# Kernel tuning notes

Hardware: AMD Instinct MI355X
Metric: run time of the kernel (lower is better)

The kernel has to match this reference:

```python
import jax, jax.numpy as jnp
import numpy as np

NUM_ITERATIONS = 3


def _squash_over_classes(s):
    # s: [B, C, O]; original squashes over dim=2 of [B,1,C,O,1] == the class dim C
    norm_sqr = jnp.sum(s * s, axis=1, keepdims=True)          # [B,1,O]
    scale = jnp.sqrt(norm_sqr) + 1e-10
    mag = norm_sqr / (1.0 + norm_sqr)
    return s * mag / scale


def setup_inputs() -> dict:
    key = jax.random.key(0)
    k1, k2 = jax.random.split(key)
    B, K, I, C, O = 256, 8, 1152, 10, 16
    x = jax.random.normal(k1, (B, K, I), dtype=jnp.float32)
    weights = jax.random.normal(k2, (I, C, O, K), dtype=jnp.float32)
    return {"x": x, "weights": weights}


def reference(x, weights):
    # x: [B, K, I]; weights: [I, C, O, K]
    B = x.shape[0]
    I, C = weights.shape[0], weights.shape[1]
    u = jnp.swapaxes(x, 1, 2)                                  # [B, I, K]
    # prediction vectors u_hat_{j|i}: [B, I, C, O]
    u_j_i = jnp.einsum('icok,bik->bico', weights, u)
    b = jnp.zeros((I, C), dtype=x.dtype)                       # routing logits (shared over batch)
    out = None
    for _ in range(NUM_ITERATIONS):
        c = jax.nn.softmax(b, axis=0)                          # softmax over input capsules I
        s = jnp.einsum('ic,bico->bco', c, u_j_i)               # weighted sum over I -> [B, C, O]
        out = _squash_over_classes(s)                          # [B, C, O]
        # agreement: <u_hat, v>, mean over batch -> [I, C]
        agr = jnp.einsum('bico,bco->ic', u_j_i, out) / B
        b = b + agr
    return out[..., None]                                      # [B, C, O, 1] matches out.squeeze(1)
```

## Files before the change

kernel.cpp:

```cpp
#include <hip/hip_runtime.h>

#define B 256
#define KDIM 8
#define IDIM 1152
#define CDIM 10
#define CO 160
#define IK 9216
#define NPART 6
#define AIT 6

typedef __bf16 bf16x8 __attribute__((ext_vector_type(8)));
typedef unsigned short ushort8 __attribute__((ext_vector_type(8)));
typedef float f32x4 __attribute__((ext_vector_type(4)));

__device__ __forceinline__ unsigned short f2bf(float f) {
  unsigned u = __float_as_uint(f);
  unsigned r = u + 0x7fff + ((u >> 16) & 1);
  return (unsigned short)(r >> 16);
}

union U8B8 { ushort8 u; bf16x8 h; };


__global__ void __launch_bounds__(256) k_prep(const float* __restrict__ x,
                                              const float* __restrict__ W,
                                              unsigned short* __restrict__ XbP,
                                              unsigned short* __restrict__ XkP,
                                              unsigned short* __restrict__ WqP,
                                              float* __restrict__ logits) {
  const int bid = blockIdx.x;
  const int t = threadIdx.x;
  if (bid < 288) {
    __shared__ float tf[KDIM * 1056];
    const int i0 = (bid % 36) * 32;
    const int b0 = (bid / 36) * 32;
    const int tx = t & 31, ty = t >> 5;
#pragma unroll
    for (int r = 0; r < 4; ++r) {
      int b = b0 + ty + r * 8;
#pragma unroll
      for (int k = 0; k < 8; ++k)
        tf[k * 1056 + (ty + r * 8) * 33 + tx] =
            x[((size_t)b * KDIM + k) * IDIM + i0 + tx];
    }
    __syncthreads();
#pragma unroll
    for (int r = 0; r < 4; ++r) {
      int idx = r * 256 + t;
      int bth = idx >> 9, kc8 = (idx >> 6) & 7, lq = (idx >> 4) & 3, lr = idx & 15;
      ushort8 v;
#pragma unroll
      for (int e = 0; e < 8; ++e)
        v[e] = f2bf(tf[e * 1056 + (bth * 16 + lr) * 33 + kc8 * 4 + lq]);
      int bt = (b0 >> 4) + bth;
      int kc = (i0 >> 2) + kc8;
      *reinterpret_cast<ushort8*>(
          &XbP[(((size_t)bt * 288 + kc) * 64 + lq * 16 + lr) * 8]) = v;
    }
    {
      const int bh = b0 >> 6, kc = (b0 >> 5) & 1;
#pragma unroll
      for (int r = 0; r < 4; ++r) {
        int idx = r * 256 + t;
        int il = idx >> 5, k = (idx >> 2) & 7, lql = idx & 3;
        int i = i0 + il;
        int bx = i / 6, r6 = i - bx * 6;
        int w = r6 >> 1, lr = (r6 & 1) * 8 + k;
        ushort8 v;
#pragma unroll
        for (int e = 0; e < 8; ++e)
          v[e] = f2bf(tf[k * 1056 + (lql * 8 + e) * 33 + il]);
        *reinterpret_cast<ushort8*>(
            &XkP[((((size_t)(bx * 3 + w) * 4 + bh) * 2 + kc) * 64 + lql * 16 + lr) * 8]) = v;
      }
    }
  } else {
    const int bz = bid - 288;
    const int i0 = bz * 16;
    const int ii = t >> 4, lr = t & 15;
    const int i = i0 + ii;
    const int kc = i >> 2, lq = i & 3;
#pragma unroll
    for (int c = 0; c < CDIM; ++c) {
      const float* src = &W[(size_t)i * 1280 + c * 128 + lr * 8];
      float4 w0 = *(const float4*)src;
      float4 w1 = *(const float4*)(src + 4);
      ushort8 v;
      v[0] = f2bf(w0.x); v[1] = f2bf(w0.y); v[2] = f2bf(w0.z); v[3] = f2bf(w0.w);
      v[4] = f2bf(w1.x); v[5] = f2bf(w1.y); v[6] = f2bf(w1.z); v[7] = f2bf(w1.w);
      *reinterpret_cast<ushort8*>(
          &WqP[(((size_t)c * 288 + kc) * 64 + lq * 16 + lr) * 8]) = v;
    }
    if (bz < 45) logits[bz * 256 + t] = 0.f;
  }
}

template <bool UNI>
__global__ void __launch_bounds__(256) k_s(const float* __restrict__ logits,
                                           const unsigned short* __restrict__ WqP,
                                           const unsigned short* __restrict__ XbP,
                                           float* __restrict__ s_part) {
  const int c = blockIdx.x, bt4 = blockIdx.y, g = blockIdx.z;
  const int t = threadIdx.x, w = t >> 6, l = t & 63;
  const int lr = l & 15, lq = l >> 4;
  const int s = g * 4 + w;

  __shared__ float red[3 * 1088];

  float qreg[12];
  if constexpr (UNI) {
#pragma unroll
    for (int t9 = 0; t9 < 12; ++t9) qreg[t9] = 1.f / (float)IDIM;
  } else {
    __shared__ float cls[IDIM];
    __shared__ float red4[4];
    float m = -1e30f;
    for (int i = t; i < IDIM; i += 256) {
      float v = logits[i * CDIM + c];
      cls[i] = v;
      m = fmaxf(m, v);
    }
#pragma unroll
    for (int off = 32; off; off >>= 1) m = fmaxf(m, __shfl_xor(m, off));
    if ((t & 63) == 0) red4[t >> 6] = m;
    __syncthreads();
    m = fmaxf(fmaxf(red4[0], red4[1]), fmaxf(red4[2], red4[3]));
    __syncthreads();
    float ps = 0.f;
    for (int i = t; i < IDIM; i += 256) {
      float e = expf(cls[i] - m);
      cls[i] = e;
      ps += e;
    }
#pragma unroll
    for (int off = 32; off; off >>= 1) ps += __shfl_xor(ps, off);
    if ((t & 63) == 0) red4[t >> 6] = ps;
    __syncthreads();
    const float rinv = 1.f / (red4[0] + red4[1] + red4[2] + red4[3]);
#pragma unroll
    for (int t9 = 0; t9 < 12; ++t9)
      qreg[t9] = cls[(s * 12 + t9) * 4 + lq] * rinv;
  }

  f32x4 acc[4];
#pragma unroll
  for (int j = 0; j < 4; ++j) acc[j] = (f32x4){0.f, 0.f, 0.f, 0.f};

  const unsigned short* Ap  = &WqP[(size_t)c * 147456 + l * 8];
  const unsigned short* Bp0 = &XbP[(size_t)(bt4 * 4 + 0) * 147456 + l * 8];
  const unsigned short* Bp1 = &XbP[(size_t)(bt4 * 4 + 1) * 147456 + l * 8];
  const unsigned short* Bp2 = &XbP[(size_t)(bt4 * 4 + 2) * 147456 + l * 8];
  const unsigned short* Bp3 = &XbP[(size_t)(bt4 * 4 + 3) * 147456 + l * 8];

#pragma unroll 4
  for (int t9 = 0; t9 < 12; ++t9) {
    const int off = (s * 12 + t9) * 512;
    ushort8 av = *reinterpret_cast<const ushort8*>(Ap + off);
    U8B8 b0; b0.u = *reinterpret_cast<const ushort8*>(Bp0 + off);
    U8B8 b1; b1.u = *reinterpret_cast<const ushort8*>(Bp1 + off);
    U8B8 b2; b2.u = *reinterpret_cast<const ushort8*>(Bp2 + off);
    U8B8 b3; b3.u = *reinterpret_cast<const ushort8*>(Bp3 + off);
    U8B8 a;
#pragma unroll
    for (int e = 0; e < 8; ++e) {
      float f = __uint_as_float((unsigned)av[e] << 16) * qreg[t9];
      a.u[e] = f2bf(f);
    }
    acc[0] = __builtin_amdgcn_mfma_f32_16x16x32_bf16(a.h, b0.h, acc[0], 0, 0, 0);
    acc[1] = __builtin_amdgcn_mfma_f32_16x16x32_bf16(a.h, b1.h, acc[1], 0, 0, 0);
    acc[2] = __builtin_amdgcn_mfma_f32_16x16x32_bf16(a.h, b2.h, acc[2], 0, 0, 0);
    acc[3] = __builtin_amdgcn_mfma_f32_16x16x32_bf16(a.h, b3.h, acc[3], 0, 0, 0);
  }

  if (w) {
#pragma unroll
    for (int j = 0; j < 4; ++j)
#pragma unroll
      for (int j2 = 0; j2 < 4; ++j2)
        red[(w - 1) * 1088 + l * 17 + j * 4 + j2] = acc[j][j2];
  }
  __syncthreads();
  if (w == 0) {
#pragma unroll
    for (int r = 0; r < 3; ++r)
#pragma unroll
      for (int j = 0; j < 4; ++j)
#pragma unroll
        for (int j2 = 0; j2 < 4; ++j2)
          acc[j][j2] += red[r * 1088 + l * 17 + j * 4 + j2];
#pragma unroll
    for (int j = 0; j < 4; ++j)
#pragma unroll
      for (int j2 = 0; j2 < 4; ++j2)
        s_part[((size_t)g * B + bt4 * 64 + j * 16 + lr) * CO + c * 16 + lq * 4 + j2] =
            acc[j][j2];
  }
}

__global__ void __launch_bounds__(256) k_sqm(const float* __restrict__ s_part,
                                             unsigned short* __restrict__ outP) {
  const int t = threadIdx.x;
  const int b0 = blockIdx.x * 8;
  __shared__ float sq[8][160];
  __shared__ float fo[8][16];
  float vv[8];
  if (t < CO) {
#pragma unroll
    for (int bi = 0; bi < 8; ++bi) {
      float sv = 0.f;
#pragma unroll
      for (int p = 0; p < NPART; ++p)
        sv += s_part[((size_t)p * B + b0 + bi) * CO + t];
      vv[bi] = sv;
      sq[bi][t] = sv * sv;
    }
  }
  __syncthreads();
  if (t < 128) {
    int bi = t >> 4, o = t & 15;
    float ns = 0.f;
#pragma unroll
    for (int c = 0; c < CDIM; ++c) ns += sq[bi][c * 16 + o];
    fo[bi][o] = (ns / (1.f + ns)) / (sqrtf(ns) + 1e-10f);
  }
  __syncthreads();
  if (t < CO) {
    const int nt = t >> 4, lr = t & 15;
    const int bh = b0 >> 6, kc = (b0 >> 5) & 1, lq = (b0 >> 3) & 3;
    ushort8 v;
#pragma unroll
    for (int bi = 0; bi < 8; ++bi) v[bi] = f2bf(vv[bi] * fo[bi][t & 15]);
    *reinterpret_cast<ushort8*>(
        &outP[((((size_t)bh * 10 + nt) * 2 + kc) * 4 + lq) * 128 + lr * 8]) = v;
  }
}

__global__ void __launch_bounds__(256) k_sqf(const float* __restrict__ s_part,
                                             float* __restrict__ out) {
  const int t = threadIdx.x;
  const int b0 = blockIdx.x * 8;
  __shared__ float sq[8][160];
  __shared__ float fo[8][16];
  float vv[8];
  if (t < CO) {
#pragma unroll
    for (int bi = 0; bi < 8; ++bi) {
      float sv = 0.f;
#pragma unroll
      for (int p = 0; p < NPART; ++p)
        sv += s_part[((size_t)p * B + b0 + bi) * CO + t];
      vv[bi] = sv;
      sq[bi][t] = sv * sv;
    }
  }
  __syncthreads();
  if (t < 128) {
    int bi = t >> 4, o = t & 15;
    float ns = 0.f;
#pragma unroll
    for (int c = 0; c < CDIM; ++c) ns += sq[bi][c * 16 + o];
    fo[bi][o] = (ns / (1.f + ns)) / (sqrtf(ns) + 1e-10f);
  }
  __syncthreads();
  if (t < CO) {
#pragma unroll
    for (int bi = 0; bi < 8; ++bi)
      out[(size_t)(b0 + bi) * CO + t] = vv[bi] * fo[bi][t & 15];
  }
}

__global__ void __launch_bounds__(256) k_agr(const float* __restrict__ W,
                                             const unsigned short* __restrict__ XkP,
                                             const unsigned short* __restrict__ outP,
                                             float* __restrict__ logits) {
  const int bx = blockIdx.x;
  const int bh = blockIdx.y;
  const int t = threadIdx.x, w = t >> 6, l = t & 63;
  const int lr = l & 15, lq = l >> 4;
  __shared__ __align__(16) float yl[CO][52];

  if (w < 3) {
    f32x4 acc[10];
#pragma unroll
    for (int nt = 0; nt < 10; ++nt) acc[nt] = (f32x4){0.f, 0.f, 0.f, 0.f};
    const unsigned short* Ap = &XkP[(((size_t)(bx * 3 + w) * 4 + bh) * 1024) + l * 8];
    const unsigned short* Bp = &outP[(size_t)bh * 10240 + l * 8];
#pragma unroll
    for (int kc = 0; kc < 2; ++kc) {
      U8B8 a; a.u = *reinterpret_cast<const ushort8*>(Ap + kc * 512);
#pragma unroll
      for (int nt = 0; nt < 10; ++nt) {
        U8B8 bv;
        bv.u = *reinterpret_cast<const ushort8*>(Bp + nt * 1024 + kc * 512);
        acc[nt] = __builtin_amdgcn_mfma_f32_16x16x32_bf16(a.h, bv.h, acc[nt], 0, 0, 0);
      }
    }
#pragma unroll
    for (int nt = 0; nt < 10; ++nt)
#pragma unroll
      for (int j = 0; j < 4; ++j)
        yl[nt * 16 + lr][w * 16 + lq * 4 + j] = acc[nt][j];
  }
  __syncthreads();

  if (t < 120) {
    const int ii = t / 20, rem = t % 20, cc = rem >> 1, oh = rem & 1;
    const float* Wp = &W[((size_t)(bx * AIT + ii) * CDIM + cc) * 128 + oh * 64];
    float sum = 0.f;
#pragma unroll
    for (int o = 0; o < 8; ++o) {
      float4 w0 = *(const float4*)(&Wp[o * 8]);
      float4 w1 = *(const float4*)(&Wp[o * 8 + 4]);
      const float* yr = &yl[cc * 16 + oh * 8 + o][ii * 8];
      float4 y0 = *(const float4*)(&yr[0]);
      float4 y1 = *(const float4*)(&yr[4]);
      sum += w0.x * y0.x + w0.y * y0.y + w0.z * y0.z + w0.w * y0.w
           + w1.x * y1.x + w1.y * y1.y + w1.z * y1.z + w1.w * y1.w;
    }
    sum += __shfl_xor(sum, 1);
    if (oh == 0)
      atomicAdd(&logits[(bx * AIT + ii) * CDIM + cc], sum * (1.f / (float)B));
  }
}

extern "C" void kernel_launch(void* const* d_in, const int* in_sizes, int n_in,
                              void* d_out, int out_size, void* d_ws, size_t ws_size,
                              hipStream_t stream) {
  const float* x = (const float*)d_in[0];
  const float* W = (const float*)d_in[1];
  float* out = (float*)d_out;

  float* logits = (float*)d_ws;
  float* s_part = logits + IDIM * CDIM;
  unsigned short* XbP = (unsigned short*)(s_part + (size_t)NPART * B * CO);
  unsigned short* XkP = XbP + (size_t)B * IK;
  unsigned short* WqP = XkP + (size_t)IK * B;
  unsigned short* outP = WqP + (size_t)CO * IK;

  k_prep<<<360, 256, 0, stream>>>(x, W, XbP, XkP, WqP, logits);

  for (int it = 0; it < 3; ++it) {
    if (it == 0)
      k_s<true><<<dim3(CDIM, 4, NPART), 256, 0, stream>>>(logits, WqP, XbP, s_part);
    else
      k_s<false><<<dim3(CDIM, 4, NPART), 256, 0, stream>>>(logits, WqP, XbP, s_part);
    if (it < 2) {
      k_sqm<<<32, 256, 0, stream>>>(s_part, outP);
      k_agr<<<dim3(IDIM / AIT, 4), 256, 0, stream>>>(W, XkP, outP, logits);
    } else {
      k_sqf<<<32, 256, 0, stream>>>(s_part, out);
    }
  }
}
```

Before: 68.28 us.

## Fuse squash into k_s via last-block atomic counter; prescale weights by 1/I

```diff
diff --git a/kernel.cpp b/kernel.cpp
--- a/kernel.cpp
+++ b/kernel.cpp
@@ -20,6 +20,16 @@
 }
 
 union U8B8 { ushort8 u; bf16x8 h; };
+union U64F2 { unsigned long long u; float f[2]; };
+
+__device__ __forceinline__ void st64_llc(void* p, unsigned long long v) {
+  __hip_atomic_store((unsigned long long*)p, v, __ATOMIC_RELAXED,
+                     __HIP_MEMORY_SCOPE_AGENT);
+}
+__device__ __forceinline__ unsigned long long ld64_llc(const void* p) {
+  return __hip_atomic_load((unsigned long long*)p, __ATOMIC_RELAXED,
+                           __HIP_MEMORY_SCOPE_AGENT);
+}
 
 
 __global__ void __launch_bounds__(256) k_prep(const float* __restrict__ x,
@@ -27,7 +37,8 @@
                                               unsigned short* __restrict__ XbP,
                                               unsigned short* __restrict__ XkP,
                                               unsigned short* __restrict__ WqP,
-                                              float* __restrict__ logits) {
+                                              float* __restrict__ logits,
+                                              int* __restrict__ cnt) {
   const int bid = blockIdx.x;
   const int t = threadIdx.x;
   if (bid < 288) {
@@ -80,40 +91,46 @@
     const int ii = t >> 4, lr = t & 15;
     const int i = i0 + ii;
     const int kc = i >> 2, lq = i & 3;
+    const float sc = 1.f / (float)IDIM;
 #pragma unroll
     for (int c = 0; c < CDIM; ++c) {
       const float* src = &W[(size_t)i * 1280 + c * 128 + lr * 8];
       float4 w0 = *(const float4*)src;
       float4 w1 = *(const float4*)(src + 4);
       ushort8 v;
-      v[0] = f2bf(w0.x); v[1] = f2bf(w0.y); v[2] = f2bf(w0.z); v[3] = f2bf(w0.w);
-      v[4] = f2bf(w1.x); v[5] = f2bf(w1.y); v[6] = f2bf(w1.z); v[7] = f2bf(w1.w);
+      v[0] = f2bf(w0.x * sc); v[1] = f2bf(w0.y * sc);
+      v[2] = f2bf(w0.z * sc); v[3] = f2bf(w0.w * sc);
+      v[4] = f2bf(w1.x * sc); v[5] = f2bf(w1.y * sc);
+      v[6] = f2bf(w1.z * sc); v[7] = f2bf(w1.w * sc);
       *reinterpret_cast<ushort8*>(
           &WqP[(((size_t)c * 288 + kc) * 64 + lq * 16 + lr) * 8]) = v;
     }
     if (bz < 45) logits[bz * 256 + t] = 0.f;
-  }
-}
-
-template <bool UNI>
+    if (bz == 45 && t < 16) cnt[t] = 0;
+  }
+}
+
+template <int MODE>
 __global__ void __launch_bounds__(256) k_s(const float* __restrict__ logits,
                                            const unsigned short* __restrict__ WqP,
                                            const unsigned short* __restrict__ XbP,
-                                           float* __restrict__ s_part) {
+                                           float* __restrict__ s_part,
+                                           unsigned short* __restrict__ outP,
+                                           float* __restrict__ out,
+                                           int* __restrict__ cnt) {
   const int c = blockIdx.x, bt4 = blockIdx.y, g = blockIdx.z;
   const int t = threadIdx.x, w = t >> 6, l = t & 63;
   const int lr = l & 15, lq = l >> 4;
   const int s = g * 4 + w;
 
-  __shared__ float red[3 * 1088];
+  __shared__ __align__(16) unsigned char smem[45064];
+  float* red = (float*)(smem) + IDIM + 4;
+  int* islast = (int*)(smem + 45056);
 
   float qreg[12];
-  if constexpr (UNI) {
-#pragma unroll
-    for (int t9 = 0; t9 < 12; ++t9) qreg[t9] = 1.f / (float)IDIM;
-  } else {
-    __shared__ float cls[IDIM];
-    __shared__ float red4[4];
+  if constexpr (MODE != 0) {
+    float* cls = (float*)smem;
+    float* red4 = cls + IDIM;
     float m = -1e30f;
     for (int i = t; i < IDIM; i += 256) {
       float v = logits[i * CDIM + c];
@@ -136,10 +153,11 @@
     for (int off = 32; off; off >>= 1) ps += __shfl_xor(ps, off);
     if ((t & 63) == 0) red4[t >> 6] = ps;
     __syncthreads();
-    const float rinv = 1.f / (red4[0] + red4[1] + red4[2] + red4[3]);
+    const float rinv = (float)IDIM / (red4[0] + red4[1] + red4[2] + red4[3]);
 #pragma unroll
     for (int t9 = 0; t9 < 12; ++t9)
       qreg[t9] = cls[(s * 12 + t9) * 4 + lq] * rinv;
+    __syncthreads();
   }
 
   f32x4 acc[4];
@@ -161,10 +179,14 @@
     U8B8 b2; b2.u = *reinterpret_cast<const ushort8*>(Bp2 + off);
     U8B8 b3; b3.u = *reinterpret_cast<const ushort8*>(Bp3 + off);
     U8B8 a;
-#pragma unroll
-    for (int e = 0; e < 8; ++e) {
-      float f = __uint_as_float((unsigned)av[e] << 16) * qreg[t9];
-      a.u[e] = f2bf(f);
+    if constexpr (MODE == 0) {
+      a.u = av;
+    } else {
+#pragma unroll
+      for (int e = 0; e < 8; ++e) {
+        float f = __uint_as_float((unsigned)av[e] << 16) * qreg[t9];
+        a.u[e] = f2bf(f);
+      }
     }
     acc[0] = __builtin_amdgcn_mfma_f32_16x16x32_bf16(a.h, b0.h, acc[0], 0, 0, 0);
     acc[1] = __builtin_amdgcn_mfma_f32_16x16x32_bf16(a.h, b1.h, acc[1], 0, 0, 0);
@@ -189,83 +211,68 @@
         for (int j2 = 0; j2 < 4; ++j2)
           acc[j][j2] += red[r * 1088 + l * 17 + j * 4 + j2];
 #pragma unroll
-    for (int j = 0; j < 4; ++j)
-#pragma unroll
-      for (int j2 = 0; j2 < 4; ++j2)
-        s_part[((size_t)g * B + bt4 * 64 + j * 16 + lr) * CO + c * 16 + lq * 4 + j2] =
-            acc[j][j2];
-  }
-}
-
-__global__ void __launch_bounds__(256) k_sqm(const float* __restrict__ s_part,
-                                             unsigned short* __restrict__ outP) {
-  const int t = threadIdx.x;
-  const int b0 = blockIdx.x * 8;
-  __shared__ float sq[8][160];
-  __shared__ float fo[8][16];
-  float vv[8];
-  if (t < CO) {
-#pragma unroll
-    for (int bi = 0; bi < 8; ++bi) {
-      float sv = 0.f;
-#pragma unroll
-      for (int p = 0; p < NPART; ++p)
-        sv += s_part[((size_t)p * B + b0 + bi) * CO + t];
-      vv[bi] = sv;
-      sq[bi][t] = sv * sv;
-    }
-  }
-  __syncthreads();
-  if (t < 128) {
-    int bi = t >> 4, o = t & 15;
+    for (int j = 0; j < 4; ++j) {
+      union { f32x4 f; unsigned long long u[2]; } cv;
+      cv.f = acc[j];
+      float* dp = &s_part[((size_t)(bt4 * 6 + g) * 64 + j * 16 + lr) * CO +
+                          c * 16 + lq * 4];
+      st64_llc(dp, cv.u[0]);
+      st64_llc(dp + 2, cv.u[1]);
+    }
+  }
+  __syncthreads();
+  if (t == 0) {
+    int old = atomicAdd(&cnt[MODE * 4 + bt4], 1);
+    *islast = (old == 59);
+  }
+  __syncthreads();
+  if (!*islast) return;
+
+  float* sq = (float*)smem;
+  float* fo = (float*)(smem + 40960);
+  for (int task = t; task < 64 * 80; task += 256) {
+    int bl = task / 80, p = task % 80;
+    const float* sp = &s_part[((size_t)(bt4 * 6) * 64 + bl) * CO + p * 2];
+    float a0 = 0.f, a1 = 0.f;
+#pragma unroll
+    for (int gg = 0; gg < 6; ++gg) {
+      U64F2 cv2; cv2.u = ld64_llc(sp + (size_t)gg * 64 * CO);
+      a0 += cv2.f[0];
+      a1 += cv2.f[1];
+    }
+    sq[bl * 160 + p * 2] = a0;
+    sq[bl * 160 + p * 2 + 1] = a1;
+  }
+  __syncthreads();
+  for (int task = t; task < 1024; task += 256) {
+    int bl = task >> 4, o = task & 15;
     float ns = 0.f;
 #pragma unroll
-    for (int c = 0; c < CDIM; ++c) ns += sq[bi][c * 16 + o];
-    fo[bi][o] = (ns / (1.f + ns)) / (sqrtf(ns) + 1e-10f);
-  }
-  __syncthreads();
-  if (t < CO) {
-    const int nt = t >> 4, lr = t & 15;
-    const int bh = b0 >> 6, kc = (b0 >> 5) & 1, lq = (b0 >> 3) & 3;
-    ushort8 v;
-#pragma unroll
-    for (int bi = 0; bi < 8; ++bi) v[bi] = f2bf(vv[bi] * fo[bi][t & 15]);
-    *reinterpret_cast<ushort8*>(
-        &outP[((((size_t)bh * 10 + nt) * 2 + kc) * 4 + lq) * 128 + lr * 8]) = v;
-  }
-}
-
-__global__ void __launch_bounds__(256) k_sqf(const float* __restrict__ s_part,
-                                             float* __restrict__ out) {
-  const int t = threadIdx.x;
-  const int b0 = blockIdx.x * 8;
-  __shared__ float sq[8][160];
-  __shared__ float fo[8][16];
-  float vv[8];
-  if (t < CO) {
-#pragma unroll
-    for (int bi = 0; bi < 8; ++bi) {
-      float sv = 0.f;
-#pragma unroll
-      for (int p = 0; p < NPART; ++p)
-        sv += s_part[((size_t)p * B + b0 + bi) * CO + t];
-      vv[bi] = sv;
-      sq[bi][t] = sv * sv;
-    }
-  }
-  __syncthreads();
-  if (t < 128) {
-    int bi = t >> 4, o = t & 15;
-    float ns = 0.f;
-#pragma unroll
-    for (int c = 0; c < CDIM; ++c) ns += sq[bi][c * 16 + o];
-    fo[bi][o] = (ns / (1.f + ns)) / (sqrtf(ns) + 1e-10f);
-  }
-  __syncthreads();
-  if (t < CO) {
-#pragma unroll
-    for (int bi = 0; bi < 8; ++bi)
-      out[(size_t)(b0 + bi) * CO + t] = vv[bi] * fo[bi][t & 15];
+    for (int cc = 0; cc < CDIM; ++cc) {
+      float v = sq[bl * 160 + cc * 16 + o];
+      ns += v * v;
+    }
+    fo[bl * 16 + o] = (ns / (1.f + ns)) / (sqrtf(ns) + 1e-10f);
+  }
+  __syncthreads();
+  if constexpr (MODE == 2) {
+    for (int task = t; task < 64 * 160; task += 256) {
+      int bl = task / 160, co = task % 160;
+      out[(size_t)(bt4 * 64 + bl) * CO + co] = sq[bl * 160 + co] * fo[bl * 16 + (co & 15)];
+    }
+  } else {
+    for (int task = t; task < 1280; task += 256) {
+      int nt = task / 128, r = task % 128;
+      int kc = r >> 6, lq2 = (r >> 4) & 3, lr2 = r & 15;
+      ushort8 v;
+#pragma unroll
+      for (int e = 0; e < 8; ++e) {
+        int bl = kc * 32 + lq2 * 8 + e;
+        v[e] = f2bf(sq[bl * 160 + nt * 16 + lr2] * fo[bl * 16 + lr2]);
+      }
+      *reinterpret_cast<ushort8*>(
+          &outP[((((size_t)bt4 * 10 + nt) * 2 + kc) * 4 + lq2) * 128 + lr2 * 8]) = v;
+    }
   }
 }
 
@@ -336,19 +343,14 @@
   unsigned short* XkP = XbP + (size_t)B * IK;
   unsigned short* WqP = XkP + (size_t)IK * B;
   unsigned short* outP = WqP + (size_t)CO * IK;
-
-  k_prep<<<360, 256, 0, stream>>>(x, W, XbP, XkP, WqP, logits);
-
-  for (int it = 0; it < 3; ++it) {
-    if (it == 0)
-      k_s<true><<<dim3(CDIM, 4, NPART), 256, 0, stream>>>(logits, WqP, XbP, s_part);
-    else
-      k_s<false><<<dim3(CDIM, 4, NPART), 256, 0, stream>>>(logits, WqP, XbP, s_part);
-    if (it < 2) {
-      k_sqm<<<32, 256, 0, stream>>>(s_part, outP);
-      k_agr<<<dim3(IDIM / AIT, 4), 256, 0, stream>>>(W, XkP, outP, logits);
-    } else {
-      k_sqf<<<32, 256, 0, stream>>>(s_part, out);
-    }
-  }
-}
+  int* cnt = (int*)(outP + (size_t)CO * B);
+
+  k_prep<<<360, 256, 0, stream>>>(x, W, XbP, XkP, WqP, logits, cnt);
+
+  dim3 gs(CDIM, 4, NPART);
+  k_s<0><<<gs, 256, 0, stream>>>(logits, WqP, XbP, s_part, outP, out, cnt);
+  k_agr<<<dim3(IDIM / AIT, 4), 256, 0, stream>>>(W, XkP, outP, logits);
+  k_s<1><<<gs, 256, 0, stream>>>(logits, WqP, XbP, s_part, outP, out, cnt);
+  k_agr<<<dim3(IDIM / AIT, 4), 256, 0, stream>>>(W, XkP, outP, logits);
+  k_s<2><<<gs, 256, 0, stream>>>(logits, WqP, XbP, s_part, outP, out, cnt);
+}
```

Measured after the change: 99.14 us. 1.45x slower.
